# Performance work log

Measured on AMD Instinct MI355X. Metric: run time of the kernel, lower is better.

Reference implementation:

```python
import jax, jax.numpy as jnp
import numpy as np

N_QUBITS = 4
N_LAYERS = 2
DIM = 2 ** N_QUBITS  # 16
B = 262144


def _cnot_perm(c, t):
    # wire 0 is the most significant bit (pennylane default.qubit convention)
    idx = np.arange(DIM)
    cb = (idx >> (N_QUBITS - 1 - c)) & 1
    return idx ^ (cb << (N_QUBITS - 1 - t))

# all-pairs CNOTs (i, j) for i < j, applied once per layer
CNOT_PERMS = [jnp.asarray(_cnot_perm(i, j)) for i in range(N_QUBITS) for j in range(i + 1, N_QUBITS)]


def _rx(t):
    c = jnp.cos(t / 2).astype(jnp.complex64)
    s = jnp.sin(t / 2).astype(jnp.complex64)
    return jnp.stack([jnp.stack([c, -1j * s], -1), jnp.stack([-1j * s, c], -1)], -2)


def _ry(t):
    c = jnp.cos(t / 2).astype(jnp.complex64)
    s = jnp.sin(t / 2).astype(jnp.complex64)
    return jnp.stack([jnp.stack([c, -s], -1), jnp.stack([s, c], -1)], -2)


def _rz(t):
    e = jnp.exp(-1j * t.astype(jnp.complex64) / 2)
    z = jnp.zeros_like(e)
    return jnp.stack([jnp.stack([e, z], -1), jnp.stack([z, jnp.conj(e)], -1)], -2)


def _apply_1q(state, gate, wire):
    # state: [B, 2,2,2,2]; gate: [2,2] (shared) or [B,2,2] (per-sample)
    ax = 1 + wire
    s = jnp.moveaxis(state, ax, -1)
    if gate.ndim == 2:
        s = jnp.einsum('b...i,ji->b...j', s, gate)
    else:
        s = jnp.einsum('b...i,bji->b...j', s, gate)
    return jnp.moveaxis(s, -1, ax)


def _circuit(x, qw):
    # x: [B, 4] rotation angles; qw: [24] circuit weights. Returns <Z_0>: [B]
    b = x.shape[0]
    state = jnp.zeros((b, DIM), jnp.complex64).at[:, 0].set(1.0)
    state = state.reshape((b,) + (2,) * N_QUBITS)
    for i in range(N_QUBITS):
        state = _apply_1q(state, _rx(x[:, i]), i)
        state = _apply_1q(state, _rz(x[:, i]), i)
    for layer in range(N_LAYERS):
        for i in range(N_QUBITS):
            state = _apply_1q(state, _ry(qw[layer * N_QUBITS + i]), i)
            state = _apply_1q(state, _rz(qw[layer * N_QUBITS + i + N_QUBITS]), i)
        flat = state.reshape(b, DIM)
        for p in CNOT_PERMS:
            flat = flat[:, p]
        state = flat.reshape((b,) + (2,) * N_QUBITS)
        for i in range(N_QUBITS):
            state = _apply_1q(state, _rx(qw[layer * N_QUBITS + i + 2 * N_QUBITS]), i)
    probs = jnp.abs(state.reshape(b, DIM)) ** 2
    zvec = jnp.where(jnp.arange(DIM) < DIM // 2, 1.0, -1.0).astype(probs.dtype)
    return probs @ zvec


def _mlp(q, W1, b1, W2, b2, W3, b3, W4, b4):
    h = jax.nn.relu(q @ W1.T + b1)
    h = jax.nn.relu(h @ W2.T + b2)
    h = jax.nn.relu(h @ W3.T + b3)
    return jax.nn.sigmoid(h @ W4.T + b4)


def setup_inputs() -> dict:
    key = jax.random.key(0)
    ks = jax.random.split(key, 10)
    def lin(k, fo, fi):
        bound = 1.0 / np.sqrt(fi)
        k1, k2 = jax.random.split(k)
        return (jax.random.uniform(k1, (fo, fi), jnp.float32, -bound, bound),
                jax.random.uniform(k2, (fo,), jnp.float32, -bound, bound))
    W1, b1 = lin(ks[2], 32, 1)
    W2, b2 = lin(ks[3], 16, 32)
    W3, b3 = lin(ks[4], 8, 16)
    W4, b4 = lin(ks[5], 1, 8)
    return {
        'x': jax.random.normal(ks[0], (B, N_QUBITS), jnp.float32),
        'qw': jax.random.normal(ks[1], (N_LAYERS * N_QUBITS * 3,), jnp.float32),
        'W1': W1, 'b1': b1, 'W2': W2, 'b2': b2,
        'W3': W3, 'b3': b3, 'W4': W4, 'b4': b4,
    }


def reference(x, qw, W1, b1, W2, b2, W3, b3, W4, b4):
    q = _circuit(x, qw)[:, None]  # [B, 1] quantum expectation values
    return _mlp(q, W1, b1, W2, b2, W3, b3, W4, b4)
```

## Files before the change

### kernel.cpp

```cpp
#include <hip/hip_runtime.h>
#include <math.h>

#define DIM 16

__global__ void qnn_setup(const float* __restrict__ qw, float* __restrict__ ws) {
  int w = threadIdx.x;
  if (w >= 4) return;
  float a = qw[0 + w];
  float b = qw[4 + w];
  float e0 = qw[8 + w];
  float c = qw[4 + w];
  float d = qw[8 + w];
  float e1 = qw[12 + w];

  ws[w * 4 + 0] = cosf(0.5f * a);
  ws[w * 4 + 1] = sinf(0.5f * a);
  ws[w * 4 + 2] = cosf(0.5f * b);
  ws[w * 4 + 3] = sinf(0.5f * b);

  float cc = cosf(0.5f * c), sc = sinf(0.5f * c);
  float ce = cosf(0.5f * e0), se = sinf(0.5f * e0);
  float m00r = cc * ce, m00i =  sc * se;
  float m01r = -sc * ce, m01i = -cc * se;
  float m10r =  sc * ce, m10i = -cc * se;
  float m11r =  cc * ce, m11i = -sc * se;
  float cd = cosf(0.5f * d), sd = sinf(0.5f * d);
  float* u = ws + 16 + w * 8;
  u[0] = cd * m00r + sd * m00i;  u[1] = cd * m00i - sd * m00r;
  u[2] = cd * m01r + sd * m01i;  u[3] = cd * m01i - sd * m01r;
  u[4] = cd * m10r - sd * m10i;  u[5] = cd * m10i + sd * m10r;
  u[6] = cd * m11r - sd * m11i;  u[7] = cd * m11i + sd * m11r;

  ws[48 + w * 2 + 0] = cosf(0.5f * e1);
  ws[48 + w * 2 + 1] = sinf(0.5f * e1);
}

__device__ __forceinline__ void cmul(float ar, float ai, float br, float bi,
                                     float& cr, float& ci) {
  cr = ar * br - ai * bi;
  ci = ar * bi + ai * br;
}

template <int TB>
__device__ __forceinline__ void apply_u(float (&sr)[DIM], float (&si)[DIM],
                                        float u00r, float u00i, float u01r, float u01i,
                                        float u10r, float u10i, float u11r, float u11i) {
#pragma unroll
  for (int i = 0; i < DIM; ++i) {
    if (i & TB) continue;
    const int j = i | TB;
    float ar = sr[i], ai = si[i], br = sr[j], bi = si[j];
    float nr = u00r * ar - u00i * ai + u01r * br - u01i * bi;
    float ni = u00r * ai + u00i * ar + u01r * bi + u01i * br;
    float mr = u10r * ar - u10i * ai + u11r * br - u11i * bi;
    float mi = u10r * ai + u10i * ar + u11r * bi + u11i * br;
    sr[i] = nr; si[i] = ni; sr[j] = mr; si[j] = mi;
  }
}

template <int TB>
__device__ __forceinline__ void apply_rx(float (&sr)[DIM], float (&si)[DIM],
                                         float cx, float sx) {
#pragma unroll
  for (int i = 0; i < DIM; ++i) {
    if (i & TB) continue;
    const int j = i | TB;
    float a0r = sr[i], a0i = si[i], a1r = sr[j], a1i = si[j];
    sr[i] = cx * a0r + sx * a1i;
    si[i] = cx * a0i - sx * a1r;
    sr[j] = cx * a1r + sx * a0i;
    si[j] = cx * a1i - sx * a0r;
  }
}

template <int CB, int TB>
__device__ __forceinline__ void apply_cnot(float (&sr)[DIM], float (&si)[DIM]) {
#pragma unroll
  for (int i = 0; i < DIM; ++i) {
    if (!(i & CB)) continue;
    if (i & TB) continue;
    const int j = i | TB;
    float tr = sr[i], ti = si[i];
    sr[i] = sr[j]; si[i] = si[j];
    sr[j] = tr;    si[j] = ti;
  }
}

__global__ __launch_bounds__(256) void qnn_kernel(
    const float* __restrict__ x, const float* __restrict__ ws,
    const float* __restrict__ W1, const float* __restrict__ b1,
    const float* __restrict__ W2, const float* __restrict__ b2,
    const float* __restrict__ W3, const float* __restrict__ b3,
    const float* __restrict__ W4, const float* __restrict__ b4,
    float* __restrict__ out, int B) {
  int b = blockIdx.x * blockDim.x + threadIdx.x;
  if (b >= B) return;

  float4 xv = reinterpret_cast<const float4*>(x)[b];
  float xs[4] = {xv.x, xv.y, xv.z, xv.w};

  float ur[4][2], ui[4][2];
#pragma unroll
  for (int w = 0; w < 4; ++w) {
    float s, c;
    __sincosf(0.5f * xs[w], &s, &c);
    float v0r0 = c * c, v0i0 = -c * s;
    float v0r1 = s * s, v0i1 = -c * s;
    float cy = ws[w * 4 + 0], sy = ws[w * 4 + 1];
    float cz = ws[w * 4 + 2], sz = ws[w * 4 + 3];
    float t0r = cy * v0r0 - sy * v0r1, t0i = cy * v0i0 - sy * v0i1;
    float t1r = sy * v0r0 + cy * v0r1, t1i = sy * v0i0 + cy * v0i1;
    ur[w][0] = cz * t0r + sz * t0i;  ui[w][0] = cz * t0i - sz * t0r;
    ur[w][1] = cz * t1r - sz * t1i;  ui[w][1] = cz * t1i + sz * t1r;
  }

  float a01r[4], a01i[4], a23r[4], a23i[4];
#pragma unroll
  for (int i0 = 0; i0 < 2; ++i0)
#pragma unroll
    for (int i1 = 0; i1 < 2; ++i1) {
      cmul(ur[0][i0], ui[0][i0], ur[1][i1], ui[1][i1], a01r[i0 * 2 + i1], a01i[i0 * 2 + i1]);
      cmul(ur[2][i0], ui[2][i0], ur[3][i1], ui[3][i1], a23r[i0 * 2 + i1], a23i[i0 * 2 + i1]);
    }
  float sr[DIM], si[DIM];
#pragma unroll
  for (int i = 0; i < DIM; ++i)
    cmul(a01r[i >> 2], a01i[i >> 2], a23r[i & 3], a23i[i & 3], sr[i], si[i]);

  apply_cnot<8, 4>(sr, si);
  apply_cnot<8, 2>(sr, si);
  apply_cnot<8, 1>(sr, si);
  apply_cnot<4, 2>(sr, si);
  apply_cnot<4, 1>(sr, si);
  apply_cnot<2, 1>(sr, si);

#define APPLY_U(WIRE, TB)                                                   \
  apply_u<TB>(sr, si, ws[16 + WIRE * 8 + 0], ws[16 + WIRE * 8 + 1],         \
              ws[16 + WIRE * 8 + 2], ws[16 + WIRE * 8 + 3],                 \
              ws[16 + WIRE * 8 + 4], ws[16 + WIRE * 8 + 5],                 \
              ws[16 + WIRE * 8 + 6], ws[16 + WIRE * 8 + 7]);
  APPLY_U(0, 8)
  APPLY_U(1, 4)
  APPLY_U(2, 2)
  APPLY_U(3, 1)
#undef APPLY_U

  apply_cnot<8, 4>(sr, si);
  apply_cnot<8, 2>(sr, si);
  apply_cnot<8, 1>(sr, si);
  apply_cnot<4, 2>(sr, si);
  apply_cnot<4, 1>(sr, si);
  apply_cnot<2, 1>(sr, si);

  apply_rx<8>(sr, si, ws[48 + 0], ws[49 + 0]);
  apply_rx<4>(sr, si, ws[48 + 2], ws[49 + 2]);
  apply_rx<2>(sr, si, ws[48 + 4], ws[49 + 4]);
  apply_rx<1>(sr, si, ws[48 + 6], ws[49 + 6]);

  float q = 0.f;
#pragma unroll
  for (int i = 0; i < DIM; ++i) {
    float p = fmaf(sr[i], sr[i], si[i] * si[i]);
    q += (i < 8) ? p : -p;
  }

  float h1[32];
#pragma unroll
  for (int j = 0; j < 32; ++j) h1[j] = fmaxf(0.f, fmaf(q, W1[j], b1[j]));

  float h2[16];
#pragma unroll
  for (int k = 0; k < 16; ++k) {
    float acc = b2[k];
#pragma unroll
    for (int j = 0; j < 32; ++j) acc = fmaf(W2[k * 32 + j], h1[j], acc);
    h2[k] = fmaxf(0.f, acc);
  }

  float h3[8];
#pragma unroll
  for (int k = 0; k < 8; ++k) {
    float acc = b3[k];
#pragma unroll
    for (int j = 0; j < 16; ++j) acc = fmaf(W3[k * 16 + j], h2[j], acc);
    h3[k] = fmaxf(0.f, acc);
  }

  float acc = b4[0];
#pragma unroll
  for (int j = 0; j < 8; ++j) acc = fmaf(W4[j], h3[j], acc);

  out[b] = 1.f / (1.f + __expf(-acc));
}

extern "C" void kernel_launch(void* const* d_in, const int* in_sizes, int n_in,
                              void* d_out, int out_size, void* d_ws, size_t ws_size,
                              hipStream_t stream) {
  const float* x  = (const float*)d_in[0];
  const float* qw = (const float*)d_in[1];
  const float* W1 = (const float*)d_in[2];
  const float* b1 = (const float*)d_in[3];
  const float* W2 = (const float*)d_in[4];
  const float* b2 = (const float*)d_in[5];
  const float* W3 = (const float*)d_in[6];
  const float* b3 = (const float*)d_in[7];
  const float* W4 = (const float*)d_in[8];
  const float* b4 = (const float*)d_in[9];
  float* out = (float*)d_out;
  float* ws  = (float*)d_ws;

  qnn_setup<<<1, 64, 0, stream>>>(qw, ws);

  const int B = in_sizes[0] / 4;
  const int block = 256;
  const int grid = (B + block - 1) / block;
  qnn_kernel<<<grid, block, 0, stream>>>(x, ws, W1, b1, W2, b2, W3, b3, W4, b4,
                                         out, B);
}
```

Baseline: 89.56 us.

## Replace per-sample MLP with interpolated LUT and fold final RX into expectation

Precomputes the scalar-input MLP on a 4097-point grid over q in [-1,1] in the setup kernel and has the main kernel linearly interpolate it, removing roughly 700 FMAs per sample. The final RX layer is folded analytically into <Z0> as cos·<Z> + sin·<Y> on wire 0, dropping four gate applications. This trades exact MLP evaluation for interpolation error bounded by grid spacing.

```diff
diff --git a/kernel.cpp b/kernel.cpp
--- a/kernel.cpp
+++ b/kernel.cpp
@@ -2,37 +2,73 @@
 #include <math.h>
 
 #define DIM 16
-
-__global__ void qnn_setup(const float* __restrict__ qw, float* __restrict__ ws) {
-  int w = threadIdx.x;
-  if (w >= 4) return;
-  float a = qw[0 + w];
-  float b = qw[4 + w];
-  float e0 = qw[8 + w];
-  float c = qw[4 + w];
-  float d = qw[8 + w];
-  float e1 = qw[12 + w];
-
-  ws[w * 4 + 0] = cosf(0.5f * a);
-  ws[w * 4 + 1] = sinf(0.5f * a);
-  ws[w * 4 + 2] = cosf(0.5f * b);
-  ws[w * 4 + 3] = sinf(0.5f * b);
-
-  float cc = cosf(0.5f * c), sc = sinf(0.5f * c);
-  float ce = cosf(0.5f * e0), se = sinf(0.5f * e0);
-  float m00r = cc * ce, m00i =  sc * se;
-  float m01r = -sc * ce, m01i = -cc * se;
-  float m10r =  sc * ce, m10i = -cc * se;
-  float m11r =  cc * ce, m11i = -sc * se;
-  float cd = cosf(0.5f * d), sd = sinf(0.5f * d);
-  float* u = ws + 16 + w * 8;
-  u[0] = cd * m00r + sd * m00i;  u[1] = cd * m00i - sd * m00r;
-  u[2] = cd * m01r + sd * m01i;  u[3] = cd * m01i - sd * m01r;
-  u[4] = cd * m10r - sd * m10i;  u[5] = cd * m10i + sd * m10r;
-  u[6] = cd * m11r - sd * m11i;  u[7] = cd * m11i + sd * m11r;
-
-  ws[48 + w * 2 + 0] = cosf(0.5f * e1);
-  ws[48 + w * 2 + 1] = sinf(0.5f * e1);
+#define LUT_N 4096
+
+__global__ void qnn_setup(const float* __restrict__ qw,
+                          const float* __restrict__ W1, const float* __restrict__ b1,
+                          const float* __restrict__ W2, const float* __restrict__ b2,
+                          const float* __restrict__ W3, const float* __restrict__ b3,
+                          const float* __restrict__ W4, const float* __restrict__ b4,
+                          float* __restrict__ ws) {
+  int gid = blockIdx.x * blockDim.x + threadIdx.x;
+
+  if (gid <= LUT_N) {
+    float q = (float)(gid - LUT_N / 2) * (2.0f / LUT_N);
+    float h1[32];
+#pragma unroll
+    for (int j = 0; j < 32; ++j) h1[j] = fmaxf(0.f, fmaf(q, W1[j], b1[j]));
+    float h2[16];
+#pragma unroll
+    for (int k = 0; k < 16; ++k) {
+      float acc = b2[k];
+#pragma unroll
+      for (int j = 0; j < 32; ++j) acc = fmaf(W2[k * 32 + j], h1[j], acc);
+      h2[k] = fmaxf(0.f, acc);
+    }
+    float h3[8];
+#pragma unroll
+    for (int k = 0; k < 8; ++k) {
+      float acc = b3[k];
+#pragma unroll
+      for (int j = 0; j < 16; ++j) acc = fmaf(W3[k * 16 + j], h2[j], acc);
+      h3[k] = fmaxf(0.f, acc);
+    }
+    float acc = b4[0];
+#pragma unroll
+    for (int j = 0; j < 8; ++j) acc = fmaf(W4[j], h3[j], acc);
+    ws[64 + gid] = 1.f / (1.f + expf(-acc));
+  } else if (gid >= 4104 && gid < 4108) {
+    int w = gid - 4104;
+    float a  = qw[0 + w];
+    float b  = qw[4 + w];
+    float e0 = qw[8 + w];
+    float c  = qw[4 + w];
+    float d  = qw[8 + w];
+    float e1 = qw[12 + w];
+
+    ws[w * 4 + 0] = cosf(0.5f * a);
+    ws[w * 4 + 1] = sinf(0.5f * a);
+    ws[w * 4 + 2] = cosf(0.5f * b);
+    ws[w * 4 + 3] = sinf(0.5f * b);
+
+    float cc = cosf(0.5f * c), sc = sinf(0.5f * c);
+    float ce = cosf(0.5f * e0), se = sinf(0.5f * e0);
+    float m00r = cc * ce,  m00i =  sc * se;
+    float m01r = -sc * ce, m01i = -cc * se;
+    float m10r =  sc * ce, m10i = -cc * se;
+    float m11r =  cc * ce, m11i = -sc * se;
+    float cd = cosf(0.5f * d), sd = sinf(0.5f * d);
+    float* u = ws + 16 + w * 8;
+    u[0] = cd * m00r + sd * m00i;  u[1] = cd * m00i - sd * m00r;
+    u[2] = cd * m01r + sd * m01i;  u[3] = cd * m01i - sd * m01r;
+    u[4] = cd * m10r - sd * m10i;  u[5] = cd * m10i + sd * m10r;
+    u[6] = cd * m11r - sd * m11i;  u[7] = cd * m11i + sd * m11r;
+
+    if (w == 0) {
+      ws[48] = cosf(e1);
+      ws[49] = sinf(e1);
+    }
+  }
 }
 
 __device__ __forceinline__ void cmul(float ar, float ai, float br, float bi,
@@ -58,21 +94,6 @@
   }
 }
 
-template <int TB>
-__device__ __forceinline__ void apply_rx(float (&sr)[DIM], float (&si)[DIM],
-                                         float cx, float sx) {
-#pragma unroll
-  for (int i = 0; i < DIM; ++i) {
-    if (i & TB) continue;
-    const int j = i | TB;
-    float a0r = sr[i], a0i = si[i], a1r = sr[j], a1i = si[j];
-    sr[i] = cx * a0r + sx * a1i;
-    si[i] = cx * a0i - sx * a1r;
-    sr[j] = cx * a1r + sx * a0i;
-    si[j] = cx * a1i - sx * a0r;
-  }
-}
-
 template <int CB, int TB>
 __device__ __forceinline__ void apply_cnot(float (&sr)[DIM], float (&si)[DIM]) {
 #pragma unroll
@@ -88,10 +109,6 @@
 
 __global__ __launch_bounds__(256) void qnn_kernel(
     const float* __restrict__ x, const float* __restrict__ ws,
-    const float* __restrict__ W1, const float* __restrict__ b1,
-    const float* __restrict__ W2, const float* __restrict__ b2,
-    const float* __restrict__ W3, const float* __restrict__ b3,
-    const float* __restrict__ W4, const float* __restrict__ b4,
     float* __restrict__ out, int B) {
   int b = blockIdx.x * blockDim.x + threadIdx.x;
   if (b >= B) return;
@@ -152,45 +169,22 @@
   apply_cnot<4, 1>(sr, si);
   apply_cnot<2, 1>(sr, si);
 
-  apply_rx<8>(sr, si, ws[48 + 0], ws[49 + 0]);
-  apply_rx<4>(sr, si, ws[48 + 2], ws[49 + 2]);
-  apply_rx<2>(sr, si, ws[48 + 4], ws[49 + 4]);
-  apply_rx<1>(sr, si, ws[48 + 6], ws[49 + 6]);
-
-  float q = 0.f;
-#pragma unroll
-  for (int i = 0; i < DIM; ++i) {
-    float p = fmaf(sr[i], sr[i], si[i] * si[i]);
-    q += (i < 8) ? p : -p;
-  }
-
-  float h1[32];
-#pragma unroll
-  for (int j = 0; j < 32; ++j) h1[j] = fmaxf(0.f, fmaf(q, W1[j], b1[j]));
-
-  float h2[16];
-#pragma unroll
-  for (int k = 0; k < 16; ++k) {
-    float acc = b2[k];
-#pragma unroll
-    for (int j = 0; j < 32; ++j) acc = fmaf(W2[k * 32 + j], h1[j], acc);
-    h2[k] = fmaxf(0.f, acc);
-  }
-
-  float h3[8];
-#pragma unroll
-  for (int k = 0; k < 8; ++k) {
-    float acc = b3[k];
-#pragma unroll
-    for (int j = 0; j < 16; ++j) acc = fmaf(W3[k * 16 + j], h2[j], acc);
-    h3[k] = fmaxf(0.f, acc);
-  }
-
-  float acc = b4[0];
-#pragma unroll
-  for (int j = 0; j < 8; ++j) acc = fmaf(W4[j], h3[j], acc);
-
-  out[b] = 1.f / (1.f + __expf(-acc));
+  float ez = 0.f, ey = 0.f;
+#pragma unroll
+  for (int i = 0; i < 8; ++i) {
+    const int j = i + 8;
+    ez += sr[i] * sr[i] + si[i] * si[i] - sr[j] * sr[j] - si[j] * si[j];
+    ey += sr[i] * si[j] - si[i] * sr[j];
+  }
+  float q = ws[48] * ez + ws[49] * (2.f * ey);
+
+  const float* lut = ws + 64;
+  float t = fmaf(q, (float)(LUT_N / 2), (float)(LUT_N / 2));
+  t = fminf(fmaxf(t, 0.f), (float)LUT_N);
+  int i0 = min((int)t, LUT_N - 1);
+  float frac = t - (float)i0;
+  float f0 = lut[i0], f1 = lut[i0 + 1];
+  out[b] = fmaf(frac, f1 - f0, f0);
 }
 
 extern "C" void kernel_launch(void* const* d_in, const int* in_sizes, int n_in,
@@ -209,11 +203,10 @@
   float* out = (float*)d_out;
   float* ws  = (float*)d_ws;
 
-  qnn_setup<<<1, 64, 0, stream>>>(qw, ws);
+  qnn_setup<<<17, 256, 0, stream>>>(qw, W1, b1, W2, b2, W3, b3, W4, b4, ws);
 
   const int B = in_sizes[0] / 4;
   const int block = 256;
   const int grid = (B + block - 1) / block;
-  qnn_kernel<<<grid, block, 0, stream>>>(x, ws, W1, b1, W2, b2, W3, b3, W4, b4,
-                                         out, B);
-}
+  qnn_kernel<<<grid, block, 0, stream>>>(x, ws, out, B);
+}
```

Result: no change. 89.51 us (-0.0%).
